# Kernel optimization log

Hardware: AMD Instinct MI355X
Metric: run time of the kernel (lower is better)

The kernel has to match this reference:

```python
import jax, jax.numpy as jnp
import numpy as np

RFF_DIM = 256
ATTENTION_SCALE = 0.1
LAMBDA_REG = 0.01
SIGMA = 1.0


def setup_inputs() -> dict:
    key = jax.random.key(0)
    k1, k2, k3 = jax.random.split(key, 3)
    N, D_IN = 262144, 64
    Z = jax.random.normal(k1, (N, D_IN), dtype=jnp.float32)
    W_rff = jax.random.normal(k2, (D_IN, RFF_DIM), dtype=jnp.float32)
    A = jax.random.normal(k3, (2 * RFF_DIM, 3), dtype=jnp.float32) * 0.01
    return {"Z": Z, "W_rff": W_rff, "A": A}


def reference(Z, W_rff, A):
    # --- RFF transform: Q = sqrt(1/R) * [cos(Z W / sigma), sin(Z W / sigma)] ---
    proj = (Z @ W_rff) / SIGMA                       # [N, R]
    Q = jnp.sqrt(1.0 / RFF_DIM) * jnp.concatenate(
        [jnp.cos(proj), jnp.sin(proj)], axis=-1)      # [N, 2R]

    N, F = Q.shape
    chunk = max(F // RFF_DIM, 1)                      # = 2 here
    n_chunks = F // chunk                             # = RFF_DIM

    # --- convexified attention over feature chunks (vectorized) ---
    Qc = Q.reshape(N, n_chunks, chunk)                # [N, K, c]
    A_mean = jnp.mean(A, axis=-1)                     # [2R]
    # per-chunk trace score: mean over batch of <Q_i, A_mean[:c]>
    scores = jnp.mean(jnp.einsum('nkc,c->nk', Qc, A_mean[:chunk]), axis=0)  # [K]
    alpha = jax.nn.softmax(scores / (ATTENTION_SCALE * np.sqrt(RFF_DIM)))   # [K]
    # per-chunk reweighting (dim-preserving recombination)
    Q_tilde = (alpha[None, :, None] * Qc).reshape(N, F)                      # [N, 2R]

    # --- small GEMM head + nuclear-norm regularizer ---
    predictions = Q_tilde @ A                          # [N, out]
    AW = jax.nn.softmax(predictions / np.sqrt(RFF_DIM), axis=-1)
    nuclear_norm = jnp.sum(jnp.linalg.svd(A, compute_uv=False))
    reg_loss = LAMBDA_REG * nuclear_norm
    return predictions, AW, reg_loss, alpha
```

## Files before the change

### kernel.cpp

```cpp
#include <hip/hip_runtime.h>
#include <math.h>

#define N_ROWS 262144
#define D_IN 64
#define RFF 256
#define NTILES (N_ROWS / 16)
#define GRID_BIG 512
#define TILES_PER_BLOCK (NTILES / GRID_BIG)
#define TILES_PER_WAVE (TILES_PER_BLOCK / 4)

#define OFF_PRED 0
#define OFF_AW (N_ROWS * 3)
#define OFF_REG (2 * N_ROWS * 3)
#define OFF_ALPHA (2 * N_ROWS * 3 + 1)

#define WS_B 512

typedef _Float16 f16x8 __attribute__((ext_vector_type(8)));
typedef float f32x4 __attribute__((ext_vector_type(4)));

__device__ __forceinline__ f32x4 mfma16(f16x8 a, f16x8 b, f32x4 c) {
    return __builtin_amdgcn_mfma_f32_16x16x32_f16(a, b, c, 0, 0, 0);
}

__device__ __forceinline__ unsigned short f32_to_bf16_rne(float x) {
    unsigned int u = __float_as_uint(x);
    unsigned int r = u + 0x7fffu + ((u >> 16) & 1u);
    return (unsigned short)(r >> 16);
}

__device__ __forceinline__ void prep_W(const float* __restrict__ W, f16x8* Bf, int t) {
#pragma unroll
    for (int q = 0; q < 8; ++q) {
        const int s = t + 256 * q;
        const int lane = s & 63;
        const int kh = (s >> 6) & 1;
        const int ct = s >> 7;
        const int k0 = kh * 32 + 8 * (lane >> 4);
        const int col = ct * 16 + (lane & 15);
        f16x8 v;
#pragma unroll
        for (int i = 0; i < 8; ++i) v[i] = (_Float16)W[(k0 + i) * RFF + col];
        Bf[(ct * 2 + kh) * 64 + lane] = v;
    }
}

__device__ __forceinline__ void stage_Z(const float* __restrict__ Z, int n0,
                                        float (*Zw)[68], int l) {
#pragma unroll
    for (int rep = 0; rep < 4; ++rep) {
        const int row = (rep >> 1) * 8 + (l >> 3);
        const int col = (rep & 1) * 32 + (l & 7) * 4;
        const float4 v = *(const float4*)(Z + (size_t)(n0 + row) * D_IN + col);
        *(float4*)&Zw[row][col] = v;
    }
    asm volatile("s_waitcnt lgkmcnt(0)" ::: "memory");
}

__device__ __forceinline__ void frags_from_lds(const float (*Zw)[68], int lr, int lh,
                                               f16x8& ah0, f16x8& al0, f16x8& ah1, f16x8& al1) {
    const float* zr = &Zw[lr][lh * 8];
    float z[16];
    *(float4*)&z[0] = *(const float4*)(zr);
    *(float4*)&z[4] = *(const float4*)(zr + 4);
    *(float4*)&z[8] = *(const float4*)(zr + 32);
    *(float4*)&z[12] = *(const float4*)(zr + 36);
#pragma unroll
    for (int i = 0; i < 8; ++i) {
        _Float16 h0 = (_Float16)z[i];
        ah0[i] = h0;
        al0[i] = (_Float16)(z[i] - (float)h0);
        _Float16 h1 = (_Float16)z[8 + i];
        ah1[i] = h1;
        al1[i] = (_Float16)(z[8 + i] - (float)h1);
    }
}

__global__ __launch_bounds__(256, 3) void k_pass1(const float* __restrict__ Z,
                                                  const float* __restrict__ W,
                                                  float* __restrict__ U) {
    __shared__ f16x8 Bf[2048];
    __shared__ float Zs[4][16][68];
    __shared__ float Ured[512];
    const int t = threadIdx.x;
    prep_W(W, Bf, t);
    Ured[t] = 0.f;
    Ured[t + 256] = 0.f;
    __syncthreads();

    const int wv = t >> 6, l = t & 63, lr = l & 15, lh = l >> 4;
    float accC[16], accS[16];
#pragma unroll
    for (int c = 0; c < 16; ++c) { accC[c] = 0.f; accS[c] = 0.f; }

    for (int tt = 0; tt < TILES_PER_WAVE; ++tt) {
        const int tile = blockIdx.x * TILES_PER_BLOCK + wv * TILES_PER_WAVE + tt;
        const int n0 = tile * 16;
        stage_Z(Z, n0, Zs[wv], l);
        f16x8 ah0, al0, ah1, al1;
        frags_from_lds(Zs[wv], lr, lh, ah0, al0, ah1, al1);
        f32x4 acc[16];
#pragma unroll
        for (int ct = 0; ct < 16; ++ct) acc[ct] = (f32x4){0.f, 0.f, 0.f, 0.f};
#pragma unroll
        for (int ct = 0; ct < 16; ++ct) {
            f16x8 b0 = Bf[(ct * 2 + 0) * 64 + l];
            f16x8 b1 = Bf[(ct * 2 + 1) * 64 + l];
            acc[ct] = mfma16(ah0, b0, acc[ct]);
            acc[ct] = mfma16(ah1, b1, acc[ct]);
            acc[ct] = mfma16(al0, b0, acc[ct]);
            acc[ct] = mfma16(al1, b1, acc[ct]);
        }
#pragma unroll
        for (int ct = 0; ct < 16; ++ct) {
#pragma unroll
            for (int r = 0; r < 4; ++r) {
                float sn, cs;
                __sincosf(acc[ct][r], &sn, &cs);
                accC[ct] += cs;
                accS[ct] += sn;
            }
        }
    }
#pragma unroll
    for (int ct = 0; ct < 16; ++ct) {
        accC[ct] += __shfl_xor(accC[ct], 16);
        accC[ct] += __shfl_xor(accC[ct], 32);
        accS[ct] += __shfl_xor(accS[ct], 16);
        accS[ct] += __shfl_xor(accS[ct], 32);
    }
    if (l < 16) {
#pragma unroll
        for (int ct = 0; ct < 16; ++ct) {
            atomicAdd(&Ured[ct * 16 + l], accC[ct] * 0.0625f);
            atomicAdd(&Ured[256 + ct * 16 + l], accS[ct] * 0.0625f);
        }
    }
    __syncthreads();
    atomicAdd(&U[t], Ured[t]);
    atomicAdd(&U[t + 256], Ured[t + 256]);
}

__global__ __launch_bounds__(256) void k_alpha(const float* __restrict__ U,
                                               const float* __restrict__ A,
                                               float* __restrict__ ws,
                                               float* __restrict__ out) {
    __shared__ float sm[256];
    __shared__ double gred[256];
    __shared__ double G6[6];
    const int k = threadIdx.x;

    const float am0 = (A[0] + A[1] + A[2]) * (1.0f / 3.0f);
    const float am1 = (A[3] + A[4] + A[5]) * (1.0f / 3.0f);
    float score = (am0 * U[2 * k] + am1 * U[2 * k + 1]) * (1.0f / (float)N_ROWS);
    float x = score * (1.0f / 1.6f);

    sm[k] = x;
    __syncthreads();
    for (int s = 128; s > 0; s >>= 1) {
        if (k < s) sm[k] = fmaxf(sm[k], sm[k + s]);
        __syncthreads();
    }
    float mx = sm[0];
    __syncthreads();
    float e = __expf(x - mx);
    sm[k] = e;
    __syncthreads();
    for (int s = 128; s > 0; s >>= 1) {
        if (k < s) sm[k] += sm[k + s];
        __syncthreads();
    }
    float al = e / sm[0];
    out[OFF_ALPHA + k] = al;
    sm[k] = al;
    __syncthreads();

    {
        const float ac = 0.0625f * sm[k >> 1];
        const float as = 0.0625f * sm[128 + (k >> 1)];
        unsigned int* BtP = (unsigned int*)(ws + WS_B);
#pragma unroll
        for (int j = 0; j < 3; ++j) {
            float bc = ac * A[k * 3 + j];
            float bs = as * A[(256 + k) * 3 + j];
            unsigned int ulo = f32_to_bf16_rne(bc);
            unsigned int uhi = f32_to_bf16_rne(bs);
            BtP[k * 3 + j] = ulo | (uhi << 16);
        }
    }

    double af[2][3];
#pragma unroll
    for (int t2 = 0; t2 < 2; ++t2)
#pragma unroll
        for (int j = 0; j < 3; ++j) af[t2][j] = (double)A[(k + t2 * 256) * 3 + j];
    const int ei[6] = {0, 0, 0, 1, 1, 2};
    const int ej[6] = {0, 1, 2, 1, 2, 2};
    for (int eidx = 0; eidx < 6; ++eidx) {
        double p = af[0][ei[eidx]] * af[0][ej[eidx]] + af[1][ei[eidx]] * af[1][ej[eidx]];
        gred[k] = p;
        __syncthreads();
        for (int s = 128; s > 0; s >>= 1) {
            if (k < s) gred[k] += gred[k + s];
            __syncthreads();
        }
        if (k == 0) G6[eidx] = gred[0];
        __syncthreads();
    }
    if (k == 0) {
        double g00 = G6[0], g01 = G6[1], g02 = G6[2], g11 = G6[3], g12 = G6[4], g22 = G6[5];
        double q = (g00 + g11 + g22) / 3.0;
        double p1 = g01 * g01 + g02 * g02 + g12 * g12;
        double p2 = (g00 - q) * (g00 - q) + (g11 - q) * (g11 - q) + (g22 - q) * (g22 - q) + 2.0 * p1;
        double nuc;
        if (p2 < 1e-300) {
            nuc = 3.0 * sqrt(fmax(q, 0.0));
        } else {
            double p = sqrt(p2 / 6.0);
            double b00 = (g00 - q) / p, b11 = (g11 - q) / p, b22 = (g22 - q) / p;
            double b01 = g01 / p, b02 = g02 / p, b12 = g12 / p;
            double detB = b00 * (b11 * b22 - b12 * b12) - b01 * (b01 * b22 - b12 * b02) +
                          b02 * (b01 * b12 - b11 * b02);
            double rr = detB / 2.0;
            rr = fmin(1.0, fmax(-1.0, rr));
            double phi = acos(rr) / 3.0;
            double e1 = q + 2.0 * p * cos(phi);
            double e3 = q + 2.0 * p * cos(phi + 2.0943951023931953);
            double e2 = 3.0 * q - e1 - e3;
            nuc = sqrt(fmax(e1, 0.0)) + sqrt(fmax(e2, 0.0)) + sqrt(fmax(e3, 0.0));
        }
        out[OFF_REG] = (float)(0.01 * nuc);
    }
}

__global__ __launch_bounds__(256, 3) void k_pass2(const float* __restrict__ Z,
                                                  const float* __restrict__ W,
                                                  const float* __restrict__ ws,
                                                  float* __restrict__ out) {
    __shared__ f16x8 Bf[2048];
    __shared__ float Zs[4][16][68];
    __shared__ unsigned int BtP[768];
    const int t = threadIdx.x;
    prep_W(W, Bf, t);
    {
        const unsigned int* src = (const unsigned int*)(ws + WS_B);
        BtP[t] = src[t];
        BtP[t + 256] = src[t + 256];
        BtP[t + 512] = src[t + 512];
    }
    __syncthreads();

    const int wv = t >> 6, l = t & 63, lr = l & 15, lh = l >> 4;

    for (int tt = 0; tt < TILES_PER_WAVE; ++tt) {
        const int tile = blockIdx.x * TILES_PER_BLOCK + wv * TILES_PER_WAVE + tt;
        const int n0 = tile * 16;
        stage_Z(Z, n0, Zs[wv], l);
        f16x8 ah0, al0, ah1, al1;
        frags_from_lds(Zs[wv], lr, lh, ah0, al0, ah1, al1);
        f32x4 acc[16];
#pragma unroll
        for (int ct = 0; ct < 16; ++ct) acc[ct] = (f32x4){0.f, 0.f, 0.f, 0.f};
#pragma unroll
        for (int ct = 0; ct < 16; ++ct) {
            f16x8 b0 = Bf[(ct * 2 + 0) * 64 + l];
            f16x8 b1 = Bf[(ct * 2 + 1) * 64 + l];
            acc[ct] = mfma16(ah0, b0, acc[ct]);
            acc[ct] = mfma16(ah1, b1, acc[ct]);
            acc[ct] = mfma16(al0, b0, acc[ct]);
            acc[ct] = mfma16(al1, b1, acc[ct]);
        }
        float pa[4][3];
#pragma unroll
        for (int r = 0; r < 4; ++r) { pa[r][0] = 0.f; pa[r][1] = 0.f; pa[r][2] = 0.f; }
#pragma unroll
        for (int ct = 0; ct < 16; ++ct) {
            const int f = ct * 16 + lr;
            unsigned int u0 = BtP[f * 3 + 0], u1 = BtP[f * 3 + 1], u2 = BtP[f * 3 + 2];
            float bc0 = __uint_as_float(u0 << 16), bs0 = __uint_as_float(u0 & 0xffff0000u);
            float bc1 = __uint_as_float(u1 << 16), bs1 = __uint_as_float(u1 & 0xffff0000u);
            float bc2 = __uint_as_float(u2 << 16), bs2 = __uint_as_float(u2 & 0xffff0000u);
#pragma unroll
            for (int r = 0; r < 4; ++r) {
                float sn, cs;
                __sincosf(acc[ct][r], &sn, &cs);
                pa[r][0] = __builtin_fmaf(cs, bc0, __builtin_fmaf(sn, bs0, pa[r][0]));
                pa[r][1] = __builtin_fmaf(cs, bc1, __builtin_fmaf(sn, bs1, pa[r][1]));
                pa[r][2] = __builtin_fmaf(cs, bc2, __builtin_fmaf(sn, bs2, pa[r][2]));
            }
        }
#pragma unroll
        for (int r = 0; r < 4; ++r)
#pragma unroll
            for (int j = 0; j < 3; ++j) {
                pa[r][j] += __shfl_xor(pa[r][j], 1);
                pa[r][j] += __shfl_xor(pa[r][j], 2);
                pa[r][j] += __shfl_xor(pa[r][j], 4);
                pa[r][j] += __shfl_xor(pa[r][j], 8);
            }
        float q0 = 0.f, q1 = 0.f, q2 = 0.f;
#pragma unroll
        for (int r = 0; r < 4; ++r)
            if (lr == r) { q0 = pa[r][0]; q1 = pa[r][1]; q2 = pa[r][2]; }
        if (lr < 4) {
            const size_t n = (size_t)n0 + 4 * lh + lr;
            out[OFF_PRED + n * 3 + 0] = q0;
            out[OFF_PRED + n * 3 + 1] = q1;
            out[OFF_PRED + n * 3 + 2] = q2;
            float x0 = q0 * 0.0625f, x1 = q1 * 0.0625f, x2 = q2 * 0.0625f;
            float m = fmaxf(x0, fmaxf(x1, x2));
            float e0 = __expf(x0 - m), e1 = __expf(x1 - m), e2 = __expf(x2 - m);
            float inv = 1.0f / (e0 + e1 + e2);
            out[OFF_AW + n * 3 + 0] = e0 * inv;
            out[OFF_AW + n * 3 + 1] = e1 * inv;
            out[OFF_AW + n * 3 + 2] = e2 * inv;
        }
    }
}

extern "C" void kernel_launch(void* const* d_in, const int* in_sizes, int n_in,
                              void* d_out, int out_size, void* d_ws, size_t ws_size,
                              hipStream_t stream) {
    const float* Z = (const float*)d_in[0];
    const float* W = (const float*)d_in[1];
    const float* A = (const float*)d_in[2];
    float* out = (float*)d_out;
    float* ws = (float*)d_ws;

    (void)hipMemsetAsync(ws, 0, 512 * sizeof(float), stream);
    hipLaunchKernelGGL(k_pass1, dim3(GRID_BIG), dim3(256), 0, stream, Z, W, ws);
    hipLaunchKernelGGL(k_alpha, dim3(1), dim3(256), 0, stream, ws, A, ws, out);
    hipLaunchKernelGGL(k_pass2, dim3(GRID_BIG), dim3(256), 0, stream, Z, W, ws, out);
}
```

Baseline: 100.5 us.

## Double-buffer Z tiles with direct global-to-LDS loads and XOR swizzle

Replaces the per-tile register-staged Z load with asynchronous global_load_lds DMA into a per-wave double buffer, prefetching the next tile while the current one is converted and multiplied. The LDS layout changes from padded rows to an XOR-swizzled 64-float row to avoid bank conflicts. This is meant to hide global load latency behind MFMA and sincos work. The larger LDS footprint drops launch bounds from 3 to 2 blocks per CU, trading occupancy for explicit prefetching.

```diff
diff --git a/kernel.cpp b/kernel.cpp
--- a/kernel.cpp
+++ b/kernel.cpp
@@ -27,6 +27,12 @@
     unsigned int u = __float_as_uint(x);
     unsigned int r = u + 0x7fffu + ((u >> 16) & 1u);
     return (unsigned short)(r >> 16);
+}
+
+__device__ __forceinline__ void gload_lds16(const float* g, float* lds) {
+    __builtin_amdgcn_global_load_lds(
+        (const __attribute__((address_space(1))) unsigned int*)g,
+        (__attribute__((address_space(3))) unsigned int*)(lds), 16, 0, 0);
 }
 
 __device__ __forceinline__ void prep_W(const float* __restrict__ W, f16x8* Bf, int t) {
@@ -45,26 +51,25 @@
     }
 }
 
-__device__ __forceinline__ void stage_Z(const float* __restrict__ Z, int n0,
-                                        float (*Zw)[68], int l) {
-#pragma unroll
-    for (int rep = 0; rep < 4; ++rep) {
-        const int row = (rep >> 1) * 8 + (l >> 3);
-        const int col = (rep & 1) * 32 + (l & 7) * 4;
-        const float4 v = *(const float4*)(Z + (size_t)(n0 + row) * D_IN + col);
-        *(float4*)&Zw[row][col] = v;
-    }
-    asm volatile("s_waitcnt lgkmcnt(0)" ::: "memory");
-}
-
-__device__ __forceinline__ void frags_from_lds(const float (*Zw)[68], int lr, int lh,
+__device__ __forceinline__ void stage_dma(const float* __restrict__ Z, int n0, int l,
+                                          float* ldsbase) {
+#pragma unroll
+    for (int m = 0; m < 4; ++m) {
+        const int row = m * 4 + (l >> 4);
+        const int gc = (l & 15) ^ (row & 7);
+        gload_lds16(Z + (size_t)(n0 + row) * D_IN + gc * 4, ldsbase + m * 256);
+    }
+}
+
+__device__ __forceinline__ void frags_from_lds(const float* bb, int lr, int lh,
                                                f16x8& ah0, f16x8& al0, f16x8& ah1, f16x8& al1) {
-    const float* zr = &Zw[lr][lh * 8];
+    const int s4 = lr & 7;
+    const float* rp = bb + lr * 64;
     float z[16];
-    *(float4*)&z[0] = *(const float4*)(zr);
-    *(float4*)&z[4] = *(const float4*)(zr + 4);
-    *(float4*)&z[8] = *(const float4*)(zr + 32);
-    *(float4*)&z[12] = *(const float4*)(zr + 36);
+    *(float4*)&z[0]  = *(const float4*)(rp + (((lh * 2 + 0) ^ s4) << 2));
+    *(float4*)&z[4]  = *(const float4*)(rp + (((lh * 2 + 1) ^ s4) << 2));
+    *(float4*)&z[8]  = *(const float4*)(rp + (((lh * 2 + 8) ^ s4) << 2));
+    *(float4*)&z[12] = *(const float4*)(rp + (((lh * 2 + 9) ^ s4) << 2));
 #pragma unroll
     for (int i = 0; i < 8; ++i) {
         _Float16 h0 = (_Float16)z[i];
@@ -76,11 +81,16 @@
     }
 }
 
-__global__ __launch_bounds__(256, 3) void k_pass1(const float* __restrict__ Z,
+#define WAITVM4() do { asm volatile("s_waitcnt vmcnt(4)" ::: "memory"); \
+                       __builtin_amdgcn_sched_barrier(0); } while (0)
+#define WAITVM0() do { asm volatile("s_waitcnt vmcnt(0)" ::: "memory"); \
+                       __builtin_amdgcn_sched_barrier(0); } while (0)
+
+__global__ __launch_bounds__(256, 2) void k_pass1(const float* __restrict__ Z,
                                                   const float* __restrict__ W,
                                                   float* __restrict__ U) {
     __shared__ f16x8 Bf[2048];
-    __shared__ float Zs[4][16][68];
+    __shared__ float Zs[4][2][1024];
     __shared__ float Ured[512];
     const int t = threadIdx.x;
     prep_W(W, Bf, t);
@@ -93,12 +103,18 @@
 #pragma unroll
     for (int c = 0; c < 16; ++c) { accC[c] = 0.f; accS[c] = 0.f; }
 
+    const int tile0 = blockIdx.x * TILES_PER_BLOCK + wv * TILES_PER_WAVE;
+    stage_dma(Z, tile0 * 16, l, &Zs[wv][0][0]);
+
     for (int tt = 0; tt < TILES_PER_WAVE; ++tt) {
-        const int tile = blockIdx.x * TILES_PER_BLOCK + wv * TILES_PER_WAVE + tt;
-        const int n0 = tile * 16;
-        stage_Z(Z, n0, Zs[wv], l);
+        if (tt + 1 < TILES_PER_WAVE) {
+            stage_dma(Z, (tile0 + tt + 1) * 16, l, &Zs[wv][(tt + 1) & 1][0]);
+            WAITVM4();
+        } else {
+            WAITVM0();
+        }
         f16x8 ah0, al0, ah1, al1;
-        frags_from_lds(Zs[wv], lr, lh, ah0, al0, ah1, al1);
+        frags_from_lds(&Zs[wv][tt & 1][0], lr, lh, ah0, al0, ah1, al1);
         f32x4 acc[16];
 #pragma unroll
         for (int ct = 0; ct < 16; ++ct) acc[ct] = (f32x4){0.f, 0.f, 0.f, 0.f};
@@ -233,12 +249,12 @@
     }
 }
 
-__global__ __launch_bounds__(256, 3) void k_pass2(const float* __restrict__ Z,
+__global__ __launch_bounds__(256, 2) void k_pass2(const float* __restrict__ Z,
                                                   const float* __restrict__ W,
                                                   const float* __restrict__ ws,
                                                   float* __restrict__ out) {
     __shared__ f16x8 Bf[2048];
-    __shared__ float Zs[4][16][68];
+    __shared__ float Zs[4][2][1024];
     __shared__ unsigned int BtP[768];
     const int t = threadIdx.x;
     prep_W(W, Bf, t);
@@ -252,12 +268,19 @@
 
     const int wv = t >> 6, l = t & 63, lr = l & 15, lh = l >> 4;
 
+    const int tile0 = blockIdx.x * TILES_PER_BLOCK + wv * TILES_PER_WAVE;
+    stage_dma(Z, tile0 * 16, l, &Zs[wv][0][0]);
+
     for (int tt = 0; tt < TILES_PER_WAVE; ++tt) {
-        const int tile = blockIdx.x * TILES_PER_BLOCK + wv * TILES_PER_WAVE + tt;
-        const int n0 = tile * 16;
-        stage_Z(Z, n0, Zs[wv], l);
+        const int n0 = (tile0 + tt) * 16;
+        if (tt + 1 < TILES_PER_WAVE) {
+            stage_dma(Z, (tile0 + tt + 1) * 16, l, &Zs[wv][(tt + 1) & 1][0]);
+            WAITVM4();
+        } else {
+            WAITVM0();
+        }
         f16x8 ah0, al0, ah1, al1;
-        frags_from_lds(Zs[wv], lr, lh, ah0, al0, ah1, al1);
+        frags_from_lds(&Zs[wv][tt & 1][0], lr, lh, ah0, al0, ah1, al1);
         f32x4 acc[16];
 #pragma unroll
         for (int ct = 0; ct < 16; ++ct) acc[ct] = (f32x4){0.f, 0.f, 0.f, 0.f};
```

New measurement: 95.98 us. 4.5% less time.
